# Kernel optimization log

Measured on AMD Instinct MI355X. Metric: run time of the kernel, lower is better.

## Reference

```python
import jax, jax.numpy as jnp
import numpy as np

S, C, HD = 2048, 3072, 128
H = C // HD  # 24 heads
EPS = 1e-6


def setup_inputs() -> dict:
    key = jax.random.key(0)
    ks = jax.random.split(key, 12)
    x = jax.random.normal(ks[0], (S, C), dtype=jnp.float32)
    rope = jax.random.normal(ks[1], (S, 1, HD // 2, 2, 2), dtype=jnp.float32)
    w = 0.02
    return {
        "x": x,
        "rope": rope,
        "wq": jax.random.normal(ks[2], (C, C), dtype=jnp.float32) * w,
        "bq": jnp.zeros((C,), dtype=jnp.float32),
        "wk": jax.random.normal(ks[3], (C, C), dtype=jnp.float32) * w,
        "bk": jnp.zeros((C,), dtype=jnp.float32),
        "wv": jax.random.normal(ks[4], (C, C), dtype=jnp.float32) * w,
        "bv": jnp.zeros((C,), dtype=jnp.float32),
        "wo": jax.random.normal(ks[5], (C, C), dtype=jnp.float32) * w,
        "bo": jnp.zeros((C,), dtype=jnp.float32),
        "qn_w": jnp.ones((HD,), dtype=jnp.float32),
        "kn_w": jnp.ones((HD,), dtype=jnp.float32),
    }


def _rmsnorm(t, w):
    # t: [S, H, HD]; normalize over last dim
    ms = jnp.mean(t * t, axis=-1, keepdims=True)
    return t * jax.lax.rsqrt(ms + EPS) * w


def _apply_rotary(t, rope):
    # t: [S, H, HD] -> [S, H, HD//2, 1, 2]; rope: [S, 1, HD//2, 2, 2]
    t_ = t.reshape(S, H, HD // 2, 1, 2)
    out = jnp.sum(rope * t_, axis=-1)  # [S, H, HD//2, 2]
    return out.reshape(S, H, HD)


def reference(x, rope, wq, bq, wk, bk, wv, bv, wo, bo, qn_w, kn_w):
    q = (x @ wq.T + bq).reshape(S, H, HD)
    k = (x @ wk.T + bk).reshape(S, H, HD)
    v = (x @ wv.T + bv).reshape(S, H, HD)
    q = _rmsnorm(q, qn_w)
    k = _rmsnorm(k, kn_w)
    q = _apply_rotary(q, rope)
    k = _apply_rotary(k, rope)
    # dense SDPA: scores [H, S, S]
    scores = jnp.einsum('shd,thd->hst', q, k) / jnp.sqrt(jnp.float32(HD))
    attn = jax.nn.softmax(scores, axis=-1)
    out = jnp.einsum('hst,thd->shd', attn, v).reshape(S, C)
    return out @ wo.T + bo
```

## Files before the change

### kernel.cpp

```cpp
#include <hip/hip_runtime.h>
#include <cstdint>
#include <cstddef>

#define SS 2048
#define CC 3072
#define HDIM 128
#define NH 24

using bf16 = __bf16;
typedef __bf16 bf16x8 __attribute__((ext_vector_type(8)));
typedef float f32x4 __attribute__((ext_vector_type(4)));

typedef const __attribute__((address_space(1))) void* gas1_cvp;
typedef __attribute__((address_space(3))) void* las3_vp;

__device__ __forceinline__ void gll16(const void* g, void* l) {
  __builtin_amdgcn_global_load_lds((gas1_cvp)g, (las3_vp)l, 16, 0, 0);
}

__device__ __forceinline__ bf16x8 cvt8(f32x4 a, f32x4 b) {
  bf16x8 r;
  r[0] = (bf16)a[0]; r[1] = (bf16)a[1]; r[2] = (bf16)a[2]; r[3] = (bf16)a[3];
  r[4] = (bf16)b[0]; r[5] = (bf16)b[1]; r[6] = (bf16)b[2]; r[7] = (bf16)b[3];
  return r;
}

#define NX ((size_t)SS * CC)
#define NW ((size_t)CC * CC)

__global__ __launch_bounds__(256)
void k_cvt(const float* __restrict__ s0, const float* __restrict__ s1,
           const float* __restrict__ s2, const float* __restrict__ s3,
           const float* __restrict__ s4, bf16* __restrict__ dst) {
  const int z = blockIdx.y;
  const float* src = (z == 0) ? s0 : (z == 1) ? s1 : (z == 2) ? s2 : (z == 3) ? s3 : s4;
  const size_t nz = (z == 0) ? NX : NW;
  const size_t base = (z == 0) ? 0 : NX + (size_t)(z - 1) * NW;
  const size_t i = ((size_t)blockIdx.x * 256 + threadIdx.x) * 8;
  if (i < nz) {
    const f32x4 a = *(const f32x4*)(src + i);
    const f32x4 b = *(const f32x4*)(src + i + 4);
    *(bf16x8*)(dst + base + i) = cvt8(a, b);
  }
}

__device__ __forceinline__ void gemm_bt_bf16(const bf16* __restrict__ A,
                                             const bf16* __restrict__ W,
                                             const float* __restrict__ bias,
                                             void* __restrict__ out,
                                             int M, int N, int K, int mode) {
  __shared__ __align__(16) bf16 As[2][128][32];
  __shared__ __align__(16) bf16 Ws[2][128][32];
  const int t = threadIdx.x, wave = t >> 6, lane = t & 63;
  const int m0 = blockIdx.y * 128, n0 = blockIdx.x * 128;
  const int wm = (wave >> 1) * 64, wn = (wave & 1) * 64;
  const int fr = lane & 15, fq = (lane >> 4) * 8;

  f32x4 acc[4][4] = {};

  for (int k0 = 0; k0 < K; k0 += 64) {
    __syncthreads();
#pragma unroll
    for (int it = 0; it < 4; ++it) {
      const int pc = wave * 4 + it;
      const int pl = pc >> 3, rb = pc & 7;
      const int row = rb * 16 + (lane >> 2);
      const int c8 = (lane & 3) * 8;
      gll16(A + (size_t)(m0 + row) * K + k0 + pl * 32 + c8,
            (char*)&As[0][0][0] + pc * 1024);
      gll16(W + (size_t)(n0 + row) * K + k0 + pl * 32 + c8,
            (char*)&Ws[0][0][0] + pc * 1024);
    }
    __syncthreads();
#pragma unroll
    for (int c = 0; c < 2; ++c) {
      bf16x8 a[4], b[4];
#pragma unroll
      for (int i = 0; i < 4; ++i) a[i] = *(const bf16x8*)&As[c][wm + i * 16 + fr][fq];
#pragma unroll
      for (int j = 0; j < 4; ++j) b[j] = *(const bf16x8*)&Ws[c][wn + j * 16 + fr][fq];
#pragma unroll
      for (int i = 0; i < 4; ++i)
#pragma unroll
        for (int j = 0; j < 4; ++j)
          acc[i][j] = __builtin_amdgcn_mfma_f32_16x16x32_bf16(a[i], b[j], acc[i][j], 0, 0, 0);
    }
  }

  const int lr4 = (lane >> 4) * 4;
#pragma unroll
  for (int i = 0; i < 4; ++i) {
#pragma unroll
    for (int j = 0; j < 4; ++j) {
      const int col = n0 + wn + j * 16 + fr;
      const float bb = bias[col];
#pragma unroll
      for (int r = 0; r < 4; ++r) {
        const int row = m0 + wm + i * 16 + lr4 + r;
        const float v = acc[i][j][r] + bb;
        if (mode == 0)
          ((bf16*)out)[((size_t)(col >> 7) * M + row) * 128 + (col & 127)] = (bf16)v;
        else if (mode == 1)
          ((bf16*)out)[(size_t)col * M + row] = (bf16)v;
        else
          ((float*)out)[(size_t)row * N + col] = v;
      }
    }
  }
}

__global__ __launch_bounds__(256, 4)
void k_gemm_qkv_b(const bf16* __restrict__ xb,
                  const bf16* __restrict__ wqb, const bf16* __restrict__ wkb,
                  const bf16* __restrict__ wvb,
                  const float* __restrict__ bq, const float* __restrict__ bk,
                  const float* __restrict__ bv,
                  bf16* __restrict__ Qo, bf16* __restrict__ Ko, bf16* __restrict__ Vo) {
  const int z = blockIdx.z;
  const bf16* W  = (z == 0) ? wqb : (z == 1) ? wkb : wvb;
  const float* B = (z == 0) ? bq : (z == 1) ? bk : bv;
  void* O        = (z == 0) ? (void*)Qo : (z == 1) ? (void*)Ko : (void*)Vo;
  gemm_bt_bf16(xb, W, B, O, SS, CC, CC, (z == 2) ? 1 : 0);
}

__global__ __launch_bounds__(256, 4)
void k_gemm_out_b(const bf16* __restrict__ A, const bf16* __restrict__ wob,
                  const float* __restrict__ bo, float* __restrict__ out) {
  gemm_bt_bf16(A, wob, bo, out, SS, CC, CC, 2);
}

template<int AF32>
__device__ __forceinline__ void gemm_core(const void* __restrict__ Ap,
                                          const float* __restrict__ W,
                                          const float* __restrict__ bias,
                                          void* __restrict__ out,
                                          int M, int N, int K, int mode) {
  __shared__ __align__(16) bf16 As[128][32];
  __shared__ __align__(16) bf16 Ws[128][32];
  const int t = threadIdx.x, wave = t >> 6, lane = t & 63;
  const int m0 = blockIdx.y * 128, n0 = blockIdx.x * 128;
  const int wm = (wave >> 1) * 64, wn = (wave & 1) * 64;
  const int fr = lane & 15, fq = (lane >> 4) * 8;
  const int pi0 = wave * 128 + lane;
  const int pi1 = pi0 + 64;
  const int row0 = pi0 >> 2, c0 = (pi0 & 3) * 8;
  const int row1 = pi1 >> 2, c1 = (pi1 & 3) * 8;

  f32x4 raf0[2], raf1[2], rw0[2], rw1[2];
  bf16x8 rab0, rab1;

  auto issue = [&](int k0) {
    if (AF32) {
      const float* A = (const float*)Ap;
      const float* p0 = A + (size_t)(m0 + row0) * K + k0 + c0;
      raf0[0] = *(const f32x4*)p0; raf0[1] = *(const f32x4*)(p0 + 4);
      const float* p1 = A + (size_t)(m0 + row1) * K + k0 + c1;
      raf1[0] = *(const f32x4*)p1; raf1[1] = *(const f32x4*)(p1 + 4);
    } else {
      const bf16* A = (const bf16*)Ap;
      rab0 = *(const bf16x8*)(A + (size_t)(m0 + row0) * K + k0 + c0);
      rab1 = *(const bf16x8*)(A + (size_t)(m0 + row1) * K + k0 + c1);
    }
    const float* q0 = W + (size_t)(n0 + row0) * K + k0 + c0;
    rw0[0] = *(const f32x4*)q0; rw0[1] = *(const f32x4*)(q0 + 4);
    const float* q1 = W + (size_t)(n0 + row1) * K + k0 + c1;
    rw1[0] = *(const f32x4*)q1; rw1[1] = *(const f32x4*)(q1 + 4);
  };

  f32x4 acc[4][4] = {};
  issue(0);
  for (int k0 = 0; k0 < K; k0 += 32) {
    __syncthreads();
    if (AF32) {
      *(bf16x8*)&As[row0][c0] = cvt8(raf0[0], raf0[1]);
      *(bf16x8*)&As[row1][c1] = cvt8(raf1[0], raf1[1]);
    } else {
      *(bf16x8*)&As[row0][c0] = rab0;
      *(bf16x8*)&As[row1][c1] = rab1;
    }
    *(bf16x8*)&Ws[row0][c0] = cvt8(rw0[0], rw0[1]);
    *(bf16x8*)&Ws[row1][c1] = cvt8(rw1[0], rw1[1]);
    __syncthreads();
    if (k0 + 32 < K) issue(k0 + 32);
    bf16x8 a[4], b[4];
#pragma unroll
    for (int i = 0; i < 4; ++i) a[i] = *(const bf16x8*)&As[wm + i * 16 + fr][fq];
#pragma unroll
    for (int j = 0; j < 4; ++j) b[j] = *(const bf16x8*)&Ws[wn + j * 16 + fr][fq];
#pragma unroll
    for (int i = 0; i < 4; ++i)
#pragma unroll
      for (int j = 0; j < 4; ++j)
        acc[i][j] = __builtin_amdgcn_mfma_f32_16x16x32_bf16(a[i], b[j], acc[i][j], 0, 0, 0);
  }

  const int lr4 = (lane >> 4) * 4;
#pragma unroll
  for (int i = 0; i < 4; ++i) {
#pragma unroll
    for (int j = 0; j < 4; ++j) {
      const int col = n0 + wn + j * 16 + fr;
      const float bb = bias[col];
#pragma unroll
      for (int r = 0; r < 4; ++r) {
        const int row = m0 + wm + i * 16 + lr4 + r;
        const float v = acc[i][j][r] + bb;
        if (mode == 0)
          ((bf16*)out)[((size_t)(col >> 7) * M + row) * 128 + (col & 127)] = (bf16)v;
        else if (mode == 1)
          ((bf16*)out)[(size_t)col * M + row] = (bf16)v;
        else
          ((float*)out)[(size_t)row * N + col] = v;
      }
    }
  }
}

__global__ __launch_bounds__(256, 2)
void k_gemm_qkv_f(const float* __restrict__ x,
                  const float* __restrict__ wq, const float* __restrict__ wk,
                  const float* __restrict__ wv,
                  const float* __restrict__ bq, const float* __restrict__ bk,
                  const float* __restrict__ bv,
                  bf16* __restrict__ Qo, bf16* __restrict__ Ko, bf16* __restrict__ Vo) {
  const int z = blockIdx.z;
  const float* W = (z == 0) ? wq : (z == 1) ? wk : wv;
  const float* B = (z == 0) ? bq : (z == 1) ? bk : bv;
  void* O        = (z == 0) ? (void*)Qo : (z == 1) ? (void*)Ko : (void*)Vo;
  gemm_core<1>(x, W, B, O, SS, CC, CC, (z == 2) ? 1 : 0);
}

__global__ __launch_bounds__(256, 2)
void k_gemm_out_f(const bf16* __restrict__ A, const float* __restrict__ wo,
                  const float* __restrict__ bo, float* __restrict__ out) {
  gemm_core<0>(A, wo, bo, out, SS, CC, CC, 2);
}

__global__ __launch_bounds__(256)
void k_norm_rope(bf16* __restrict__ Q, bf16* __restrict__ K,
                 const float* __restrict__ rope,
                 const float* __restrict__ qw, const float* __restrict__ kw) {
  const int t = threadIdx.x, wave = t >> 6, lane = t & 63;
  const int idx = blockIdx.x * 4 + wave;
  const int s = idx / NH, h = idx % NH;
  const size_t base = ((size_t)h * SS + s) * HDIM + 2 * lane;

  bf16 q2[2], k2[2];
  *(uint32_t*)q2 = *(const uint32_t*)(Q + base);
  *(uint32_t*)k2 = *(const uint32_t*)(K + base);
  const float q0 = (float)q2[0], q1 = (float)q2[1];
  const float k0 = (float)k2[0], k1 = (float)k2[1];
  float sq = q0 * q0 + q1 * q1;
  float sk = k0 * k0 + k1 * k1;
#pragma unroll
  for (int m = 1; m < 64; m <<= 1) {
    sq += __shfl_xor(sq, m);
    sk += __shfl_xor(sk, m);
  }
  const float rq = rsqrtf(sq * (1.0f / 128.0f) + 1e-6f);
  const float rk = rsqrtf(sk * (1.0f / 128.0f) + 1e-6f);

  const float qn0 = q0 * rq * qw[2 * lane], qn1 = q1 * rq * qw[2 * lane + 1];
  const float kn0 = k0 * rk * kw[2 * lane], kn1 = k1 * rk * kw[2 * lane + 1];

  const f32x4 rp = *(const f32x4*)(rope + (size_t)s * 256 + 4 * lane);
  const float r00 = rp[0], r01 = rp[1], r10 = rp[2], r11 = rp[3];

  const float SC = 0.08838834764831845f * 1.44269504088896340f;
  const float oq0 = (r00 * qn0 + r01 * qn1) * SC;
  const float oq1 = (r10 * qn0 + r11 * qn1) * SC;
  const float ok0 = r00 * kn0 + r01 * kn1;
  const float ok1 = r10 * kn0 + r11 * kn1;

  bf16 wq2[2] = {(bf16)oq0, (bf16)oq1};
  bf16 wk2[2] = {(bf16)ok0, (bf16)ok1};
  *(uint32_t*)(Q + base) = *(uint32_t*)wq2;
  *(uint32_t*)(K + base) = *(uint32_t*)wk2;
}

__global__ __launch_bounds__(128, 2)
void k_attn(const bf16* __restrict__ Q, const bf16* __restrict__ Kt,
            const bf16* __restrict__ Vt, bf16* __restrict__ Out) {
  __shared__ __align__(16) bf16 Ks[64][128];
  __shared__ __align__(16) bf16 Vs[128][64];
  __shared__ __align__(16) bf16 Ps[64][72];
  const int t = threadIdx.x, wave = t >> 6, lane = t & 63;
  const int bx = blockIdx.x;
  const int xg = bx & 7, slot = bx >> 3;
  const int h = xg * 3 + (slot >> 5);
  const int q0 = (slot & 31) * 64;
  const int fr = lane & 15, fq = (lane >> 4) * 8;
  const int g4 = lane >> 4;
  const int lr4 = (lane >> 4) * 4;
  const int wq0 = wave * 32;
  const float FM = 32.0f;

  bf16x8 aq[2][4];
#pragma unroll
  for (int qt = 0; qt < 2; ++qt)
#pragma unroll
    for (int kc = 0; kc < 4; ++kc)
      aq[qt][kc] = *(const bf16x8*)(
          Q + ((size_t)h * SS + q0 + wq0 + qt * 16 + fr) * HDIM + kc * 32 + fq);

  f32x4 oacc[2][8] = {};
  float lacc[2][4] = {};

  for (int k0 = 0; k0 < SS; k0 += 64) {
    __syncthreads();
#pragma unroll
    for (int it = 0; it < 8; ++it) {
      const int pc = wave * 8 + it;
      {
        const int row = pc * 4 + (lane >> 4);
        const int sl  = (lane & 15) ^ (row & 7);
        gll16(Kt + ((size_t)h * SS + k0 + row) * HDIM + sl * 8,
              (char*)&Ks[0][0] + pc * 1024);
      }
      {
        const int d  = pc * 8 + (lane >> 3);
        const int sl = (lane & 7) ^ (d & 7);
        gll16(Vt + ((size_t)h * HDIM + d) * SS + k0 + sl * 8,
              (char*)&Vs[0][0] + pc * 1024);
      }
    }
    __syncthreads();

    f32x4 sacc[2][4] = {};
#pragma unroll
    for (int kc = 0; kc < 4; ++kc) {
#pragma unroll
      for (int jt = 0; jt < 4; ++jt) {
        const int kp = jt * 16 + fr;
        const bf16x8 b =
            *(const bf16x8*)&Ks[kp][((((kc << 2) + g4) ^ (fr & 7)) << 3)];
        sacc[0][jt] = __builtin_amdgcn_mfma_f32_16x16x32_bf16(aq[0][kc], b, sacc[0][jt], 0, 0, 0);
        sacc[1][jt] = __builtin_amdgcn_mfma_f32_16x16x32_bf16(aq[1][kc], b, sacc[1][jt], 0, 0, 0);
      }
    }

#pragma unroll
    for (int qt = 0; qt < 2; ++qt) {
#pragma unroll
      for (int r = 0; r < 4; ++r) {
        float ps = 0.f;
#pragma unroll
        for (int jt = 0; jt < 4; ++jt) {
          const float pv = exp2f(sacc[qt][jt][r] - FM);
          ps += pv;
          Ps[wq0 + qt * 16 + lr4 + r][jt * 16 + fr] = (bf16)pv;
        }
        lacc[qt][r] += ps;
      }
    }
    asm volatile("s_waitcnt lgkmcnt(0)" ::: "memory");

#pragma unroll
    for (int kc = 0; kc < 2; ++kc) {
      const bf16x8 ap0 = *(const bf16x8*)&Ps[wq0 + fr][kc * 32 + fq];
      const bf16x8 ap1 = *(const bf16x8*)&Ps[wq0 + 16 + fr][kc * 32 + fq];
#pragma unroll
      for (int jd = 0; jd < 8; ++jd) {
        const int d = jd * 16 + fr;
        const bf16x8 b =
            *(const bf16x8*)&Vs[d][((((kc << 2) + g4) ^ (fr & 7)) << 3)];
        oacc[0][jd] = __builtin_amdgcn_mfma_f32_16x16x32_bf16(ap0, b, oacc[0][jd], 0, 0, 0);
        oacc[1][jd] = __builtin_amdgcn_mfma_f32_16x16x32_bf16(ap1, b, oacc[1][jd], 0, 0, 0);
      }
    }
  }

#pragma unroll
  for (int qt = 0; qt < 2; ++qt) {
#pragma unroll
    for (int r = 0; r < 4; ++r) {
      float l = lacc[qt][r];
      l += __shfl_xor(l, 1);
      l += __shfl_xor(l, 2);
      l += __shfl_xor(l, 4);
      l += __shfl_xor(l, 8);
      const float inv = 1.0f / l;
      const int row = q0 + wq0 + qt * 16 + lr4 + r;
#pragma unroll
      for (int jd = 0; jd < 8; ++jd) {
        const int col = h * HDIM + jd * 16 + fr;
        Out[(size_t)row * CC + col] = (bf16)(oacc[qt][jd][r] * inv);
      }
    }
  }
}

extern "C" void kernel_launch(void* const* d_in, const int* in_sizes, int n_in,
                              void* d_out, int out_size, void* d_ws, size_t ws_size,
                              hipStream_t stream) {
  const float* x    = (const float*)d_in[0];
  const float* rope = (const float*)d_in[1];
  const float* wq   = (const float*)d_in[2];
  const float* bq   = (const float*)d_in[3];
  const float* wk   = (const float*)d_in[4];
  const float* bk   = (const float*)d_in[5];
  const float* wv   = (const float*)d_in[6];
  const float* bv   = (const float*)d_in[7];
  const float* wo   = (const float*)d_in[8];
  const float* bo   = (const float*)d_in[9];
  const float* qw   = (const float*)d_in[10];
  const float* kw   = (const float*)d_in[11];

  const size_t need = (4 * NX + 4 * NW) * sizeof(bf16);
  bf16* Vt = (bf16*)d_out;

  if (ws_size >= need) {
    bf16* xb  = (bf16*)d_ws;
    bf16* wqb = xb + NX;
    bf16* wkb = wqb + NW;
    bf16* wvb = wkb + NW;
    bf16* wob = wvb + NW;
    bf16* Qn  = wob + NW;
    bf16* Kn  = Qn + NX;
    bf16* Ao  = Kn + NX;

    k_cvt<<<dim3((unsigned)(NW / 2048), 5), 256, 0, stream>>>(x, wq, wk, wv, wo, xb);
    k_gemm_qkv_b<<<dim3(CC / 128, SS / 128, 3), 256, 0, stream>>>(
        xb, wqb, wkb, wvb, bq, bk, bv, Qn, Kn, Vt);
    k_norm_rope<<<dim3(SS * NH / 4), 256, 0, stream>>>(Qn, Kn, rope, qw, kw);
    k_attn<<<dim3((SS / 64) * NH), 128, 0, stream>>>(Qn, Kn, Vt, Ao);
    k_gemm_out_b<<<dim3(CC / 128, SS / 128), 256, 0, stream>>>(Ao, wob, bo, (float*)d_out);
  } else {
    bf16* Qn = (bf16*)d_ws;
    bf16* Kn = Qn + NX;
    bf16* Ao = Kn + NX;

    k_gemm_qkv_f<<<dim3(CC / 128, SS / 128, 3), 256, 0, stream>>>(
        x, wq, wk, wv, bq, bk, bv, Qn, Kn, Vt);
    k_norm_rope<<<dim3(SS * NH / 4), 256, 0, stream>>>(Qn, Kn, rope, qw, kw);
    k_attn<<<dim3((SS / 64) * NH), 128, 0, stream>>>(Qn, Kn, Vt, Ao);
    k_gemm_out_f<<<dim3(CC / 128, SS / 128), 256, 0, stream>>>(Ao, wo, bo, (float*)d_out);
  }
}
```

Measured before the change: 524.2 us.

## Keep softmax probabilities in registers by transposing QK^T MFMA operands

```diff
diff --git a/kernel.cpp b/kernel.cpp
--- a/kernel.cpp
+++ b/kernel.cpp
@@ -283,7 +283,6 @@
             const bf16* __restrict__ Vt, bf16* __restrict__ Out) {
   __shared__ __align__(16) bf16 Ks[64][128];
   __shared__ __align__(16) bf16 Vs[128][64];
-  __shared__ __align__(16) bf16 Ps[64][72];
   const int t = threadIdx.x, wave = t >> 6, lane = t & 63;
   const int bx = blockIdx.x;
   const int xg = bx & 7, slot = bx >> 3;
@@ -291,7 +290,6 @@
   const int q0 = (slot & 31) * 64;
   const int fr = lane & 15, fq = (lane >> 4) * 8;
   const int g4 = lane >> 4;
-  const int lr4 = (lane >> 4) * 4;
   const int wq0 = wave * 32;
   const float FM = 32.0f;
 
@@ -304,7 +302,7 @@
           Q + ((size_t)h * SS + q0 + wq0 + qt * 16 + fr) * HDIM + kc * 32 + fq);
 
   f32x4 oacc[2][8] = {};
-  float lacc[2][4] = {};
+  float lacc[2] = {0.f, 0.f};
 
   for (int k0 = 0; k0 < SS; k0 += 64) {
     __syncthreads();
@@ -312,9 +310,11 @@
     for (int it = 0; it < 8; ++it) {
       const int pc = wave * 8 + it;
       {
-        const int row = pc * 4 + (lane >> 4);
-        const int sl  = (lane & 15) ^ (row & 7);
-        gll16(Kt + ((size_t)h * SS + k0 + row) * HDIM + sl * 8,
+        const int s  = pc * 4 + (lane >> 4);
+        const int kp = 32 * ((s >> 4) & 1) + 8 * ((s >> 2) & 3)
+                     + 4 * (s >> 5) + (s & 3);
+        const int sl = (lane & 15) ^ (s & 7);
+        gll16(Kt + ((size_t)h * SS + k0 + kp) * HDIM + sl * 8,
               (char*)&Ks[0][0] + pc * 1024);
       }
       {
@@ -331,56 +331,60 @@
     for (int kc = 0; kc < 4; ++kc) {
 #pragma unroll
       for (int jt = 0; jt < 4; ++jt) {
-        const int kp = jt * 16 + fr;
         const bf16x8 b =
-            *(const bf16x8*)&Ks[kp][((((kc << 2) + g4) ^ (fr & 7)) << 3)];
-        sacc[0][jt] = __builtin_amdgcn_mfma_f32_16x16x32_bf16(aq[0][kc], b, sacc[0][jt], 0, 0, 0);
-        sacc[1][jt] = __builtin_amdgcn_mfma_f32_16x16x32_bf16(aq[1][kc], b, sacc[1][jt], 0, 0, 0);
-      }
-    }
-
+            *(const bf16x8*)&Ks[jt * 16 + fr][((((kc << 2) + g4) ^ (fr & 7)) << 3)];
+        sacc[0][jt] = __builtin_amdgcn_mfma_f32_16x16x32_bf16(b, aq[0][kc], sacc[0][jt], 0, 0, 0);
+        sacc[1][jt] = __builtin_amdgcn_mfma_f32_16x16x32_bf16(b, aq[1][kc], sacc[1][jt], 0, 0, 0);
+      }
+    }
+
+    bf16x8 ap[2][2];
 #pragma unroll
     for (int qt = 0; qt < 2; ++qt) {
-#pragma unroll
-      for (int r = 0; r < 4; ++r) {
-        float ps = 0.f;
-#pragma unroll
-        for (int jt = 0; jt < 4; ++jt) {
-          const float pv = exp2f(sacc[qt][jt][r] - FM);
-          ps += pv;
-          Ps[wq0 + qt * 16 + lr4 + r][jt * 16 + fr] = (bf16)pv;
+      float pv[4][4];
+      float ps = 0.f;
+#pragma unroll
+      for (int jt = 0; jt < 4; ++jt)
+#pragma unroll
+        for (int r = 0; r < 4; ++r) {
+          pv[jt][r] = exp2f(sacc[qt][jt][r] - FM);
+          ps += pv[jt][r];
         }
-        lacc[qt][r] += ps;
-      }
-    }
-    asm volatile("s_waitcnt lgkmcnt(0)" ::: "memory");
+      lacc[qt] += ps;
+#pragma unroll
+      for (int kc = 0; kc < 2; ++kc) {
+        bf16x8 a;
+        a[0] = (bf16)pv[kc][0];     a[1] = (bf16)pv[kc][1];
+        a[2] = (bf16)pv[kc][2];     a[3] = (bf16)pv[kc][3];
+        a[4] = (bf16)pv[2 + kc][0]; a[5] = (bf16)pv[2 + kc][1];
+        a[6] = (bf16)pv[2 + kc][2]; a[7] = (bf16)pv[2 + kc][3];
+        ap[qt][kc] = a;
+      }
+    }
 
 #pragma unroll
     for (int kc = 0; kc < 2; ++kc) {
-      const bf16x8 ap0 = *(const bf16x8*)&Ps[wq0 + fr][kc * 32 + fq];
-      const bf16x8 ap1 = *(const bf16x8*)&Ps[wq0 + 16 + fr][kc * 32 + fq];
 #pragma unroll
       for (int jd = 0; jd < 8; ++jd) {
         const int d = jd * 16 + fr;
         const bf16x8 b =
             *(const bf16x8*)&Vs[d][((((kc << 2) + g4) ^ (fr & 7)) << 3)];
-        oacc[0][jd] = __builtin_amdgcn_mfma_f32_16x16x32_bf16(ap0, b, oacc[0][jd], 0, 0, 0);
-        oacc[1][jd] = __builtin_amdgcn_mfma_f32_16x16x32_bf16(ap1, b, oacc[1][jd], 0, 0, 0);
+        oacc[0][jd] = __builtin_amdgcn_mfma_f32_16x16x32_bf16(ap[0][kc], b, oacc[0][jd], 0, 0, 0);
+        oacc[1][jd] = __builtin_amdgcn_mfma_f32_16x16x32_bf16(ap[1][kc], b, oacc[1][jd], 0, 0, 0);
       }
     }
   }
 
 #pragma unroll
   for (int qt = 0; qt < 2; ++qt) {
+    float l = lacc[qt];
+    l += __shfl_xor(l, 16);
+    l += __shfl_xor(l, 32);
+    const float linv = 1.0f / l;
 #pragma unroll
     for (int r = 0; r < 4; ++r) {
-      float l = lacc[qt][r];
-      l += __shfl_xor(l, 1);
-      l += __shfl_xor(l, 2);
-      l += __shfl_xor(l, 4);
-      l += __shfl_xor(l, 8);
-      const float inv = 1.0f / l;
-      const int row = q0 + wq0 + qt * 16 + lr4 + r;
+      const float inv = __shfl(linv, g4 * 4 + r, 16);
+      const int row = q0 + wq0 + qt * 16 + g4 * 4 + r;
 #pragma unroll
       for (int jd = 0; jd < 8; ++jd) {
         const int col = h * HDIM + jd * 16 + fr;
```

New measurement: 532.0 us. About the same (+1.5%).
